# Kernel tuning notes

Measured on AMD Instinct MI355X. Metric: run time of the kernel, lower is better.

The kernel has to match this reference:

```python
import jax, jax.numpy as jnp
import numpy as np

H = 256  # hidden_size


def setup_inputs() -> dict:
    key = jax.random.key(0)
    k1, k2, k3 = jax.random.split(key, 3)
    N, L, V, Emb = 128, 2048, 32000, 256
    X = jax.random.randint(k1, (N, L), 0, V, dtype=jnp.int64)
    E = jax.random.normal(k2, (V, Emb), dtype=jnp.float32) * 0.02
    W_w = jax.random.normal(k3, (4 * H, H + Emb), dtype=jnp.float32) * (1.0 / np.sqrt(H + Emb))
    W_b = jnp.zeros((4 * H,), dtype=jnp.float32)
    return {"X": X, "E": E, "W_w": W_w, "W_b": W_b}


def reference(X, E, W_w, W_b):
    # X: (N, L) int token ids
    N, L = X.shape
    Xe = E[X]                      # (N, L, Emb) embedded sequence
    Xe_t = jnp.swapaxes(Xe, 0, 1)  # (L, N, Emb) scan over time

    def step(carry, x_t):
        H_t, C_t = carry
        hx = jnp.concatenate([H_t, x_t], axis=1)           # (N, H+Emb)
        G = hx @ W_w.T + W_b                               # (N, 4H)
        F_g = jax.nn.sigmoid(G[:, :H])
        # NOTE: original code computes I = sigmoid(G[:, H:2H]) but never uses it
        O_g = jax.nn.sigmoid(G[:, 2 * H:3 * H])
        H_tmp = jnp.tanh(G[:, 3 * H:4 * H])
        # Faithful to source: C_t = F*C + O*H_tmp (uses O, not I)
        C_new = F_g * C_t + O_g * H_tmp
        H_new = O_g * jnp.tanh(C_new)
        return (H_new, C_new), None

    init = (jnp.zeros((N, H), Xe.dtype), jnp.zeros((N, H), Xe.dtype))
    (H_last, _), _ = jax.lax.scan(step, init, Xe_t)
    return H_last
```

## Files before the change

### kernel.cpp

```cpp
#include <hip/hip_runtime.h>
#include <hip/hip_bf16.h>

#define N_B   128
#define L_SEQ 2048
#define H_DIM 256
#define EMB   256
#define G3    768
#define G4    1024
#define WROW  512
#define V_SZ  32000


typedef unsigned short ushort_t;
typedef unsigned int   uint_t;

using f32x4  = __attribute__((ext_vector_type(4))) float;
using bf16x8 = __attribute__((ext_vector_type(8))) short;
using h2_t   = __attribute__((ext_vector_type(2))) _Float16;
using ushort4_t = __attribute__((ext_vector_type(4))) ushort_t;

__device__ __forceinline__ float bf2f(ushort_t u) {
  union { uint_t u; float f; } x; x.u = ((uint_t)u) << 16; return x.f;
}
__device__ __forceinline__ ushort_t f2bf(float f) {
  union { float f; uint_t u; } x; x.f = f;
  return (ushort_t)((x.u + 0x7fffu + ((x.u >> 16) & 1u)) >> 16);
}
__device__ __forceinline__ float rcp_f(float x) {
#if __has_builtin(__builtin_amdgcn_rcpf)
  return __builtin_amdgcn_rcpf(x);
#else
  return 1.0f / x;
#endif
}
__device__ __forceinline__ float clampf(float x, float lo, float hi) {
  return fminf(fmaxf(x, lo), hi);
}
__device__ __forceinline__ float sigmoid_f(float x) {
  x = clampf(x, -30.f, 30.f);
  return rcp_f(1.0f + __expf(-x));
}
__device__ __forceinline__ float tanh_f(float x) {
  x = clampf(x, -15.f, 15.f);
  float e = __expf(-2.0f * x);
  return (1.0f - e) * rcp_f(1.0f + e);
}
__device__ __forceinline__ float fdot2_f(h2_t a, h2_t b, float c) {
#if __has_builtin(__builtin_amdgcn_fdot2)
  return __builtin_amdgcn_fdot2(a, b, c, false);
#else
  return c + (float)a.x * (float)b.x + (float)a.y * (float)b.y;
#endif
}
__device__ __forceinline__ uint_t lane_bcast(uint_t v, int l) {
#if __has_builtin(__builtin_amdgcn_readlane)
  return (uint_t)__builtin_amdgcn_readlane((int)v, l);
#else
  return (uint_t)__shfl((int)v, l, 64);
#endif
}
__device__ __forceinline__ h2_t bfpair_to_h2(uint_t u) {
  union { uint_t u; float f; } lo, hi;
  lo.u = u << 16;
  hi.u = u & 0xffff0000u;
  h2_t r; r.x = (_Float16)lo.f; r.y = (_Float16)hi.f; return r;
}

__device__ __forceinline__ int gmap(int g) { return (g < 256) ? g : g + 256; }

__global__ void dtype_probe(const uint_t* __restrict__ Ed,
                            const uint_t* __restrict__ Xd,
                            const uint_t* __restrict__ Wd,
                            uint_t* __restrict__ flags) {
  if (threadIdx.x != 0 || blockIdx.x != 0) return;
  int saneE = 0, saneW = 0;
  for (int i = 0; i < 256; ++i) {
    uint_t le = Ed[i] & 0xffffu, ee = (le >> 7) & 0xffu;
    if (ee == 0u || (ee >= 90u && ee <= 126u)) saneE++;
    uint_t lw = Wd[i] & 0xffffu, ew = (lw >> 7) & 0xffu;
    if (ew == 0u || (ew >= 90u && ew <= 126u)) saneW++;
  }
  uint_t nz = 0u;
  for (int i = 0; i < 128; ++i) nz |= Xd[2 * i + 1];
  flags[0] = (saneE < 192) ? 1u : 0u;
  flags[1] = (nz == 0u) ? 1u : 0u;
  flags[2] = (saneW < 192) ? 1u : 0u;
}

__global__ __launch_bounds__(256) void eg_gemm(const void* __restrict__ Ein,
                                               const void* __restrict__ Wwin,
                                               const void* __restrict__ Wbin,
                                               _Float16* __restrict__ Eg,
                                               const uint_t* __restrict__ flags) {
  __shared__ __align__(16) ushort_t At[16][264];
  const int tid = threadIdx.x;
  const int v0  = blockIdx.x * 16;
  const uint_t ef32 = flags[0];
  const uint_t wf32 = flags[2];

  if (!ef32) {
    const ushort_t* E = (const ushort_t*)Ein;
#pragma unroll
    for (int i = 0; i < 2; ++i) {
      int idx = tid + i * 256;
      int row = idx >> 5, seg = idx & 31;
      const uint4* src = (const uint4*)(E + (size_t)(v0 + row) * EMB + seg * 8);
      *(uint4*)&At[row][seg * 8] = *src;
    }
  } else {
    const float* Ef = (const float*)Ein;
#pragma unroll
    for (int i = 0; i < 4; ++i) {
      int idx = tid + i * 256;
      int row = idx >> 6, seg = idx & 63;
      float4 v = *(const float4*)(Ef + (size_t)(v0 + row) * EMB + seg * 4);
      ushort4_t s;
      s.x = f2bf(v.x); s.y = f2bf(v.y); s.z = f2bf(v.z); s.w = f2bf(v.w);
      *(ushort4_t*)&At[row][seg * 4] = s;
    }
  }
  __syncthreads();

  const int lane = tid & 63, wv = tid >> 6;
  const int m = lane & 15, q = lane >> 4;

  f32x4 acc[12];
#pragma unroll
  for (int nt = 0; nt < 12; ++nt) acc[nt] = f32x4{0.f, 0.f, 0.f, 0.f};

  if (!wf32) {
    const ushort_t* Ww = (const ushort_t*)Wwin;
#pragma unroll
    for (int kt = 0; kt < 8; ++kt) {
      bf16x8 a = *(const bf16x8*)&At[m][kt * 32 + q * 8];
#pragma unroll
      for (int nt = 0; nt < 12; ++nt) {
        int g  = wv * 192 + nt * 16 + m;
        int gr = gmap(g);
        const bf16x8* bp =
            (const bf16x8*)(Ww + (size_t)gr * WROW + EMB + kt * 32 + q * 8);
        acc[nt] = __builtin_amdgcn_mfma_f32_16x16x32_bf16(a, *bp, acc[nt], 0, 0, 0);
      }
    }
  } else {
    const float* Wf = (const float*)Wwin;
#pragma unroll
    for (int kt = 0; kt < 8; ++kt) {
      bf16x8 a = *(const bf16x8*)&At[m][kt * 32 + q * 8];
#pragma unroll
      for (int nt = 0; nt < 12; ++nt) {
        int g  = wv * 192 + nt * 16 + m;
        int gr = gmap(g);
        const float* wp = Wf + (size_t)gr * WROW + EMB + kt * 32 + q * 8;
        float4 w0 = *(const float4*)(wp);
        float4 w1 = *(const float4*)(wp + 4);
        bf16x8 b;
        b[0] = (short)f2bf(w0.x); b[1] = (short)f2bf(w0.y);
        b[2] = (short)f2bf(w0.z); b[3] = (short)f2bf(w0.w);
        b[4] = (short)f2bf(w1.x); b[5] = (short)f2bf(w1.y);
        b[6] = (short)f2bf(w1.z); b[7] = (short)f2bf(w1.w);
        acc[nt] = __builtin_amdgcn_mfma_f32_16x16x32_bf16(a, b, acc[nt], 0, 0, 0);
      }
    }
  }

#pragma unroll
  for (int nt = 0; nt < 12; ++nt) {
    int g  = wv * 192 + nt * 16 + m;
    int gr = gmap(g);
    float bias = wf32 ? ((const float*)Wbin)[gr] : bf2f(((const ushort_t*)Wbin)[gr]);
#pragma unroll
    for (int j = 0; j < 4; ++j) {
      int v = v0 + q * 4 + j;
      Eg[(size_t)v * G3 + g] = (_Float16)(acc[nt][j] + bias);
    }
  }
}

__global__
__attribute__((amdgpu_flat_work_group_size(512, 512), amdgpu_waves_per_eu(2, 2)))
void lstm_rec(const int* __restrict__ Xi,
              const void* __restrict__ Wwin,
              const _Float16* __restrict__ Eg,
              float* __restrict__ out,
              const uint_t* __restrict__ flags) {
  __shared__ uint_t hbuf[2][128];
  __shared__ float  pbuf[G3];
  const int tid  = threadIdx.x;
  const int lane = tid & 63;
  const int half = tid >> 8;
  const int j    = tid & 255;
  const int n    = blockIdx.x;
  const uint_t wf32 = flags[2];
  const uint_t x64  = flags[1];

  uint_t wF[64], wO[64], wT[64];
  if (!wf32) {
    const uint_t* rF = (const uint_t*)((const ushort_t*)Wwin + (size_t)(j)       * WROW + half * 128);
    const uint_t* rO = (const uint_t*)((const ushort_t*)Wwin + (size_t)(512 + j) * WROW + half * 128);
    const uint_t* rT = (const uint_t*)((const ushort_t*)Wwin + (size_t)(768 + j) * WROW + half * 128);
#pragma unroll
    for (int d = 0; d < 64; ++d) {
      wF[d] = __builtin_bit_cast(uint_t, bfpair_to_h2(rF[d]));
      wO[d] = __builtin_bit_cast(uint_t, bfpair_to_h2(rO[d]));
      wT[d] = __builtin_bit_cast(uint_t, bfpair_to_h2(rT[d]));
    }
  } else {
    const float* rF = (const float*)Wwin + (size_t)(j)       * WROW + half * 128;
    const float* rO = (const float*)Wwin + (size_t)(512 + j) * WROW + half * 128;
    const float* rT = (const float*)Wwin + (size_t)(768 + j) * WROW + half * 128;
#pragma unroll
    for (int d = 0; d < 64; ++d) {
      float2 vF = *(const float2*)(rF + 2 * d);
      float2 vO = *(const float2*)(rO + 2 * d);
      float2 vT = *(const float2*)(rT + 2 * d);
      h2_t f, o, t2;
      f.x  = (_Float16)vF.x; f.y  = (_Float16)vF.y;
      o.x  = (_Float16)vO.x; o.y  = (_Float16)vO.y;
      t2.x = (_Float16)vT.x; t2.y = (_Float16)vT.y;
      wF[d] = __builtin_bit_cast(uint_t, f);
      wO[d] = __builtin_bit_cast(uint_t, o);
      wT[d] = __builtin_bit_cast(uint_t, t2);
    }
  }
#pragma unroll
  for (int d = 0; d < 64; ++d) {
    asm volatile("" : "+v"(wF[d]), "+v"(wO[d]), "+v"(wT[d]));
  }

  if (tid < 128) hbuf[0][tid] = 0u;

  float c = 0.f, hlast = 0.f;
  const size_t xbase = (size_t)n * L_SEQ;

  float pxF = 0.f, pxO = 0.f, pxT = 0.f;
  if (half == 0) {
    int tok0 = x64 ? Xi[xbase * 2] : Xi[xbase];
    if ((uint_t)tok0 >= (uint_t)V_SZ) tok0 = 0;
    const _Float16* e = Eg + (size_t)tok0 * G3 + j;
    pxF = (float)e[0]; pxO = (float)e[256]; pxT = (float)e[512];
  }

  int cur = 0;
  for (int t = 0; t < L_SEQ; ++t) {
    __syncthreads();

    const uint_t hv = hbuf[cur][half * 64 + lane];

    float nF = 0.f, nO = 0.f, nT = 0.f;
    if (half == 0) {
      int tp = (t + 1 < L_SEQ) ? (t + 1) : (L_SEQ - 1);
      int tok = x64 ? Xi[(xbase + tp) * 2] : Xi[xbase + tp];
      if ((uint_t)tok >= (uint_t)V_SZ) tok = 0;
      const _Float16* e = Eg + (size_t)tok * G3 + j;
      nF = (float)e[0]; nO = (float)e[256]; nT = (float)e[512];
    }

    float aF0 = 0.f, aO0 = 0.f, aT0 = 0.f;
    float aF1 = 0.f, aO1 = 0.f, aT1 = 0.f;
#pragma unroll
    for (int d = 0; d < 64; ++d) {
      h2_t hh = __builtin_bit_cast(h2_t, lane_bcast(hv, d));
      h2_t wf = __builtin_bit_cast(h2_t, wF[d]);
      h2_t wo = __builtin_bit_cast(h2_t, wO[d]);
      h2_t wt = __builtin_bit_cast(h2_t, wT[d]);
      if (d & 1) {
        aF1 = fdot2_f(wf, hh, aF1);
        aO1 = fdot2_f(wo, hh, aO1);
        aT1 = fdot2_f(wt, hh, aT1);
      } else {
        aF0 = fdot2_f(wf, hh, aF0);
        aO0 = fdot2_f(wo, hh, aO0);
        aT0 = fdot2_f(wt, hh, aT0);
      }
    }
    float aF = aF0 + aF1, aO = aO0 + aO1, aT = aT0 + aT1;

    if (half == 1) {
      pbuf[j]       = aF;
      pbuf[256 + j] = aO;
      pbuf[512 + j] = aT;
    }
    __syncthreads();

    if (half == 0) {
      aF += pbuf[j]       + pxF;
      aO += pbuf[256 + j] + pxO;
      aT += pbuf[512 + j] + pxT;
      float Fg = sigmoid_f(aF);
      float Og = sigmoid_f(aO);
      float Tg = tanh_f(aT);
      c = Fg * c + Og * Tg;
      float hv2 = Og * tanh_f(c);
      hlast = hv2;
      ((_Float16*)hbuf[cur ^ 1])[j] = (_Float16)hv2;
      pxF = nF; pxO = nO; pxT = nT;
    }
    cur ^= 1;
  }

  if (half == 0) out[(size_t)n * H_DIM + j] = hlast;
}

extern "C" void kernel_launch(void* const* d_in, const int* in_sizes, int n_in,
                              void* d_out, int out_size, void* d_ws, size_t ws_size,
                              hipStream_t stream) {
  const void* X  = d_in[0];
  const void* E  = d_in[1];
  const void* Ww = d_in[2];
  const void* Wb = d_in[3];
  for (int i = 0; i < n_in && i < 4; ++i) {
    switch (in_sizes[i]) {
      case N_B * L_SEQ: X  = d_in[i]; break;
      case V_SZ * EMB:  E  = d_in[i]; break;
      case G4 * WROW:   Ww = d_in[i]; break;
      case G4:          Wb = d_in[i]; break;
      default: break;
    }
  }
  float* out = (float*)d_out;

  uint_t*   flags = (uint_t*)d_ws;
  _Float16* Eg    = (_Float16*)((char*)d_ws + 256);

  dtype_probe<<<dim3(1), dim3(64), 0, stream>>>(
      (const uint_t*)E, (const uint_t*)X, (const uint_t*)Ww, flags);
  eg_gemm<<<dim3(V_SZ / 16), dim3(256), 0, stream>>>(E, Ww, Wb, Eg, flags);
  lstm_rec<<<dim3(N_B), dim3(512), 0, stream>>>((const int*)X, Ww, Eg, out, flags);
}
```

Baseline: 3.028 ms.

## Split recurrent hidden-dim reduction across four thread quarters with 1024-thread blocks

The recurrent LSTM kernel now splits the 256-wide hidden-state dot product across four groups of 256 threads instead of two, doubling block size to 1024. Each thread keeps 96 weight registers instead of 192 and runs half as many fdot2 steps per timestep. Three partial sums go through shared memory and are added by the first quarter. This shortens the serial per-step critical path, at the cost of more LDS traffic, a larger cross-wave reduction, and barriers across 16 waves.

```diff
diff --git a/kernel.cpp b/kernel.cpp
--- a/kernel.cpp
+++ b/kernel.cpp
@@ -18,6 +18,7 @@
 using bf16x8 = __attribute__((ext_vector_type(8))) short;
 using h2_t   = __attribute__((ext_vector_type(2))) _Float16;
 using ushort4_t = __attribute__((ext_vector_type(4))) ushort_t;
+using u32x4  = __attribute__((ext_vector_type(4))) uint_t;
 
 __device__ __forceinline__ float bf2f(ushort_t u) {
   union { uint_t u; float f; } x; x.u = ((uint_t)u) << 16; return x.f;
@@ -178,55 +179,53 @@
 }
 
 __global__
-__attribute__((amdgpu_flat_work_group_size(512, 512), amdgpu_waves_per_eu(2, 2)))
+__attribute__((amdgpu_flat_work_group_size(1024, 1024), amdgpu_waves_per_eu(4, 4)))
 void lstm_rec(const int* __restrict__ Xi,
               const void* __restrict__ Wwin,
               const _Float16* __restrict__ Eg,
               float* __restrict__ out,
               const uint_t* __restrict__ flags) {
   __shared__ uint_t hbuf[2][128];
-  __shared__ float  pbuf[G3];
+  __shared__ float  pbuf[3][G3];
   const int tid  = threadIdx.x;
   const int lane = tid & 63;
-  const int half = tid >> 8;
+  const int q4   = tid >> 8;
   const int j    = tid & 255;
   const int n    = blockIdx.x;
   const uint_t wf32 = flags[2];
   const uint_t x64  = flags[1];
 
-  uint_t wF[64], wO[64], wT[64];
+  uint_t w[96];
   if (!wf32) {
-    const uint_t* rF = (const uint_t*)((const ushort_t*)Wwin + (size_t)(j)       * WROW + half * 128);
-    const uint_t* rO = (const uint_t*)((const ushort_t*)Wwin + (size_t)(512 + j) * WROW + half * 128);
-    const uint_t* rT = (const uint_t*)((const ushort_t*)Wwin + (size_t)(768 + j) * WROW + half * 128);
-#pragma unroll
-    for (int d = 0; d < 64; ++d) {
-      wF[d] = __builtin_bit_cast(uint_t, bfpair_to_h2(rF[d]));
-      wO[d] = __builtin_bit_cast(uint_t, bfpair_to_h2(rO[d]));
-      wT[d] = __builtin_bit_cast(uint_t, bfpair_to_h2(rT[d]));
+    const ushort_t* Wb16 = (const ushort_t*)Wwin;
+#pragma unroll
+    for (int G = 0; G < 3; ++G) {
+      const int row = (G == 0) ? j : ((G == 1) ? 512 + j : 768 + j);
+      const u32x4* src = (const u32x4*)(Wb16 + (size_t)row * WROW + q4 * 64);
+#pragma unroll
+      for (int i = 0; i < 8; ++i) {
+        u32x4 v = src[i];
+#pragma unroll
+        for (int cdw = 0; cdw < 4; ++cdw)
+          w[G * 32 + i * 4 + cdw] = __builtin_bit_cast(uint_t, bfpair_to_h2(v[cdw]));
+      }
     }
   } else {
-    const float* rF = (const float*)Wwin + (size_t)(j)       * WROW + half * 128;
-    const float* rO = (const float*)Wwin + (size_t)(512 + j) * WROW + half * 128;
-    const float* rT = (const float*)Wwin + (size_t)(768 + j) * WROW + half * 128;
-#pragma unroll
-    for (int d = 0; d < 64; ++d) {
-      float2 vF = *(const float2*)(rF + 2 * d);
-      float2 vO = *(const float2*)(rO + 2 * d);
-      float2 vT = *(const float2*)(rT + 2 * d);
-      h2_t f, o, t2;
-      f.x  = (_Float16)vF.x; f.y  = (_Float16)vF.y;
-      o.x  = (_Float16)vO.x; o.y  = (_Float16)vO.y;
-      t2.x = (_Float16)vT.x; t2.y = (_Float16)vT.y;
-      wF[d] = __builtin_bit_cast(uint_t, f);
-      wO[d] = __builtin_bit_cast(uint_t, o);
-      wT[d] = __builtin_bit_cast(uint_t, t2);
-    }
-  }
-#pragma unroll
-  for (int d = 0; d < 64; ++d) {
-    asm volatile("" : "+v"(wF[d]), "+v"(wO[d]), "+v"(wT[d]));
-  }
+    const float* Wf = (const float*)Wwin;
+#pragma unroll
+    for (int G = 0; G < 3; ++G) {
+      const int row = (G == 0) ? j : ((G == 1) ? 512 + j : 768 + j);
+      const float* src = Wf + (size_t)row * WROW + q4 * 64;
+#pragma unroll
+      for (int dd = 0; dd < 32; ++dd) {
+        float2 v = *(const float2*)(src + 2 * dd);
+        h2_t p; p.x = (_Float16)v.x; p.y = (_Float16)v.y;
+        w[G * 32 + dd] = __builtin_bit_cast(uint_t, p);
+      }
+    }
+  }
+#pragma unroll
+  for (int dd = 0; dd < 96; ++dd) asm volatile("" : "+v"(w[dd]));
 
   if (tid < 128) hbuf[0][tid] = 0u;
 
@@ -234,7 +233,7 @@
   const size_t xbase = (size_t)n * L_SEQ;
 
   float pxF = 0.f, pxO = 0.f, pxT = 0.f;
-  if (half == 0) {
+  if (q4 == 0) {
     int tok0 = x64 ? Xi[xbase * 2] : Xi[xbase];
     if ((uint_t)tok0 >= (uint_t)V_SZ) tok0 = 0;
     const _Float16* e = Eg + (size_t)tok0 * G3 + j;
@@ -245,10 +244,10 @@
   for (int t = 0; t < L_SEQ; ++t) {
     __syncthreads();
 
-    const uint_t hv = hbuf[cur][half * 64 + lane];
+    const uint_t hv = hbuf[cur][q4 * 32 + (lane & 31)];
 
     float nF = 0.f, nO = 0.f, nT = 0.f;
-    if (half == 0) {
+    if (q4 == 0) {
       int tp = (t + 1 < L_SEQ) ? (t + 1) : (L_SEQ - 1);
       int tok = x64 ? Xi[(xbase + tp) * 2] : Xi[xbase + tp];
       if ((uint_t)tok >= (uint_t)V_SZ) tok = 0;
@@ -259,11 +258,11 @@
     float aF0 = 0.f, aO0 = 0.f, aT0 = 0.f;
     float aF1 = 0.f, aO1 = 0.f, aT1 = 0.f;
 #pragma unroll
-    for (int d = 0; d < 64; ++d) {
+    for (int d = 0; d < 32; ++d) {
       h2_t hh = __builtin_bit_cast(h2_t, lane_bcast(hv, d));
-      h2_t wf = __builtin_bit_cast(h2_t, wF[d]);
-      h2_t wo = __builtin_bit_cast(h2_t, wO[d]);
-      h2_t wt = __builtin_bit_cast(h2_t, wT[d]);
+      h2_t wf = __builtin_bit_cast(h2_t, w[d]);
+      h2_t wo = __builtin_bit_cast(h2_t, w[32 + d]);
+      h2_t wt = __builtin_bit_cast(h2_t, w[64 + d]);
       if (d & 1) {
         aF1 = fdot2_f(wf, hh, aF1);
         aO1 = fdot2_f(wo, hh, aO1);
@@ -276,17 +275,17 @@
     }
     float aF = aF0 + aF1, aO = aO0 + aO1, aT = aT0 + aT1;
 
-    if (half == 1) {
-      pbuf[j]       = aF;
-      pbuf[256 + j] = aO;
-      pbuf[512 + j] = aT;
+    if (q4 != 0) {
+      pbuf[q4 - 1][j]       = aF;
+      pbuf[q4 - 1][256 + j] = aO;
+      pbuf[q4 - 1][512 + j] = aT;
     }
     __syncthreads();
 
-    if (half == 0) {
-      aF += pbuf[j]       + pxF;
-      aO += pbuf[256 + j] + pxO;
-      aT += pbuf[512 + j] + pxT;
+    if (q4 == 0) {
+      aF += pbuf[0][j]       + pbuf[1][j]       + pbuf[2][j]       + pxF;
+      aO += pbuf[0][256 + j] + pbuf[1][256 + j] + pbuf[2][256 + j] + pxO;
+      aT += pbuf[0][512 + j] + pbuf[1][512 + j] + pbuf[2][512 + j] + pxT;
       float Fg = sigmoid_f(aF);
       float Og = sigmoid_f(aO);
       float Tg = tanh_f(aT);
@@ -299,7 +298,7 @@
     cur ^= 1;
   }
 
-  if (half == 0) out[(size_t)n * H_DIM + j] = hlast;
+  if (q4 == 0) out[(size_t)n * H_DIM + j] = hlast;
 }
 
 extern "C" void kernel_launch(void* const* d_in, const int* in_sizes, int n_in,
@@ -326,5 +325,5 @@
   dtype_probe<<<dim3(1), dim3(64), 0, stream>>>(
       (const uint_t*)E, (const uint_t*)X, (const uint_t*)Ww, flags);
   eg_gemm<<<dim3(V_SZ / 16), dim3(256), 0, stream>>>(E, Ww, Wb, Eg, flags);
-  lstm_rec<<<dim3(N_B), dim3(512), 0, stream>>>((const int*)X, Ww, Eg, out, flags);
-}
+  lstm_rec<<<dim3(N_B), dim3(1024), 0, stream>>>((const int*)X, Ww, Eg, out, flags);
+}
```

After: 3.003 ms. About the same (-0.8%).
